# Kernel tuning notes

Measured on AMD Instinct MI355X. Metric: run time of the kernel, lower is better.

Reference implementation:

```python
import jax, jax.numpy as jnp
import numpy as np


def _gcn_norm(edge_index, num_nodes):
    # PyG GCNConv(normalize=True): add self-loops, symmetric normalization.
    src, dst = edge_index[0], edge_index[1]
    loop = jnp.arange(num_nodes, dtype=src.dtype)
    src = jnp.concatenate([src, loop])
    dst = jnp.concatenate([dst, loop])
    ones = jnp.ones(src.shape[0], dtype=jnp.float32)
    deg = jax.ops.segment_sum(ones, dst, num_segments=num_nodes)
    dinv = jax.lax.rsqrt(jnp.maximum(deg, 1.0))  # deg >= 1 with self-loops
    norm = dinv[src] * dinv[dst]  # [E+N]
    return src, dst, norm


def _gcn_layer(x, W, b, src, dst, norm, num_nodes):
    h = x @ W                                   # [N, out]
    msg = norm[:, None] * h[src]                # [E+N, out] gather
    agg = jax.ops.segment_sum(msg, dst, num_segments=num_nodes)  # scatter-add
    return agg + b


def setup_inputs() -> dict:
    key = jax.random.key(0)
    ks = jax.random.split(key, 8)
    N, E, F = 50000, 400000, 128
    v = jax.random.normal(ks[0], (N, F), dtype=jnp.float32)
    edge_index = jax.random.randint(ks[1], (2, E), 0, N, dtype=jnp.int64)
    def glorot(k, fan_in, fan_out):
        s = jnp.sqrt(6.0 / (fan_in + fan_out))
        return jax.random.uniform(k, (fan_in, fan_out), jnp.float32, -s, s)
    return {
        "v": v,
        "edge_index": edge_index,
        "W1": glorot(ks[2], F, 128), "b1": jnp.zeros((128,), jnp.float32),
        "W2": glorot(ks[3], 128, 256), "b2": jnp.zeros((256,), jnp.float32),
        "W3": glorot(ks[4], 256, 512), "b3": jnp.zeros((512,), jnp.float32),
    }


def reference(v, edge_index, W1, b1, W2, b2, W3, b3):
    N = v.shape[0]
    src, dst, norm = _gcn_norm(edge_index, N)
    x = jax.nn.relu(_gcn_layer(v, W1, b1, src, dst, norm, N))
    x = jax.nn.relu(_gcn_layer(x, W2, b2, src, dst, norm, N))
    x = jax.nn.relu(_gcn_layer(x, W3, b3, src, dst, norm, N))
    return x
```

## Files before the change

kernel.cpp:

```cpp
#include <hip/hip_runtime.h>
#include <hip/hip_bf16.h>
#include <stdint.h>

static constexpr int NN = 50000;
static constexpr int NE = 400000;
static constexpr int NB = (NN + 1023) / 1024;

typedef __attribute__((ext_vector_type(8))) short bf16x8;
typedef __attribute__((ext_vector_type(8))) unsigned short u16x8;
typedef __attribute__((ext_vector_type(4))) float f32x4;

__device__ inline ushort f2bf(float f) {
    __hip_bfloat16 b = __float2bfloat16(f);
    return *reinterpret_cast<ushort*>(&b);
}
__device__ inline float bfu2f(ushort u) {
    unsigned x = (unsigned)u << 16;
    return __builtin_bit_cast(float, x);
}

__device__ __forceinline__ void gload16(const void* g, void* l) {
    __builtin_amdgcn_global_load_lds(
        (const __attribute__((address_space(1))) void*)g,
        (__attribute__((address_space(3))) void*)l, 16, 0, 0);
}


__global__ void k_count(const int* __restrict__ ei, unsigned* __restrict__ cnt) {
    int e = blockIdx.x * blockDim.x + threadIdx.x;
    if (e < NE) atomicAdd(&cnt[ei[NE + e]], 1u);
}

__global__ void k_dinv(const unsigned* __restrict__ cnt, float* __restrict__ dinv) {
    int i = blockIdx.x * blockDim.x + threadIdx.x;
    if (i < NN) dinv[i] = rsqrtf((float)(cnt[i] + 1u));
}


__global__ __launch_bounds__(1024) void k_scan1(const unsigned* __restrict__ cnt,
                                                unsigned* __restrict__ offs,
                                                unsigned* __restrict__ bsum) {
    __shared__ unsigned sh[1024];
    int i = blockIdx.x * 1024 + (int)threadIdx.x;
    unsigned v = (i < NN) ? cnt[i] : 0u;
    sh[threadIdx.x] = v;
    __syncthreads();
    #pragma unroll
    for (int off = 1; off < 1024; off <<= 1) {
        unsigned add = (threadIdx.x >= (unsigned)off) ? sh[threadIdx.x - off] : 0u;
        __syncthreads();
        sh[threadIdx.x] += add;
        __syncthreads();
    }
    if (i < NN) offs[i] = sh[threadIdx.x] - v;
    if (threadIdx.x == 1023) bsum[blockIdx.x] = sh[1023];
}

__global__ void k_scan2(const unsigned* __restrict__ bsum, unsigned* __restrict__ boff,
                        unsigned* __restrict__ offs) {
    if (threadIdx.x == 0) {
        unsigned acc = 0;
        for (int b = 0; b < NB; ++b) { boff[b] = acc; acc += bsum[b]; }
        offs[NN] = acc;
    }
}

__global__ __launch_bounds__(1024) void k_scan3(unsigned* __restrict__ offs,
                                                const unsigned* __restrict__ boff) {
    int i = blockIdx.x * 1024 + (int)threadIdx.x;
    if (i < NN) offs[i] += boff[blockIdx.x];
}

__global__ void k_fill(const int* __restrict__ ei, const unsigned* __restrict__ offs,
                       unsigned* __restrict__ cursor, const float* __restrict__ dinv,
                       unsigned* __restrict__ csr_src, float* __restrict__ csr_w) {
    int e = blockIdx.x * blockDim.x + threadIdx.x;
    if (e < NE) {
        int s = ei[e];
        int d = ei[NE + e];
        unsigned pos = offs[d] + atomicAdd(&cursor[d], 1u);
        csr_src[pos] = (unsigned)s;
        csr_w[pos] = dinv[s] * dinv[d];
    }
}


__global__ void k_castW(const float* __restrict__ W, ushort* __restrict__ Wt, int K, int N) {
    int i = blockIdx.x * 256 + (int)threadIdx.x;
    if (i >= K * N) return;
    int k = i / N, n = i - k * N;
    Wt[n * K + k] = f2bf(W[i]);
}


__global__ void k_castV(const float* __restrict__ v, ushort* __restrict__ vb, int n4) {
    int i = blockIdx.x * 256 + (int)threadIdx.x;
    if (i >= n4) return;
    float4 f = *reinterpret_cast<const float4*>(v + (size_t)i * 4);
    *reinterpret_cast<ushort4*>(vb + (size_t)i * 4) =
        make_ushort4(f2bf(f.x), f2bf(f.y), f2bf(f.z), f2bf(f.w));
}


template <int VEC>
__global__ __launch_bounds__(256) void k_aggregate(
        const ushort* __restrict__ x, ushort* __restrict__ y,
        const unsigned* __restrict__ offs, const unsigned* __restrict__ csr_src,
        const float* __restrict__ csr_w, const float* __restrict__ dinv) {
    const int F = 64 * VEC;
    constexpr int LPR = (VEC == 2) ? 16 : 32;
    constexpr int NEP = 64 / LPR;
    constexpr int U = 8 / NEP;
    int node = blockIdx.x * 4 + ((int)threadIdx.x >> 6);
    int lane = (int)threadIdx.x & 63;
    if (node >= NN) return;
    int h = lane / LPR;
    int sl = lane % LPR;

    float di = dinv[node];
    float sw = (h == 0) ? di * di : 0.f;
    float acc[8];
    {
        u16x8 u = *reinterpret_cast<const u16x8*>(x + (size_t)node * F + sl * 8);
        #pragma unroll
        for (int j = 0; j < 8; ++j) acc[j] = sw * bfu2f(u[j]);
    }

    unsigned beg = offs[node], end = offs[node + 1];
    unsigned e = beg + h;
    for (; e + NEP * (U - 1) < end; e += NEP * U) {
        unsigned s[U]; float w[U]; u16x8 u[U];
        #pragma unroll
        for (int k = 0; k < U; ++k) { s[k] = csr_src[e + NEP * k]; w[k] = csr_w[e + NEP * k]; }
        #pragma unroll
        for (int k = 0; k < U; ++k)
            u[k] = *reinterpret_cast<const u16x8*>(x + (size_t)s[k] * F + sl * 8);
        #pragma unroll
        for (int k = 0; k < U; ++k)
            #pragma unroll
            for (int j = 0; j < 8; ++j) acc[j] = fmaf(w[k], bfu2f(u[k][j]), acc[j]);
    }
    for (; e < end; e += NEP) {
        unsigned s0 = csr_src[e];
        float w0 = csr_w[e];
        u16x8 u0 = *reinterpret_cast<const u16x8*>(x + (size_t)s0 * F + sl * 8);
        #pragma unroll
        for (int j = 0; j < 8; ++j) acc[j] = fmaf(w0, bfu2f(u0[j]), acc[j]);
    }

    #pragma unroll
    for (int j = 0; j < 8; ++j) {
        acc[j] += __shfl_xor(acc[j], 32);
        if constexpr (LPR == 16) acc[j] += __shfl_xor(acc[j], 16);
    }

    if (h == 0) {
        ushort hh[8];
        #pragma unroll
        for (int j = 0; j < 8; ++j) hh[j] = f2bf(acc[j]);
        *reinterpret_cast<u16x8*>(y + (size_t)node * F + sl * 8) =
            *reinterpret_cast<u16x8*>(hh);
    }
}


template <int NT, int SC, bool OUTB>
__global__ __launch_bounds__(256, 4) void k_gemm7(
        const ushort* __restrict__ Ah, const ushort* __restrict__ Wt,
        const float* __restrict__ bias, void* __restrict__ Cout, int M, int N) {
    constexpr int K = NT * 32;
    constexpr int CHT = (NT > 2) ? 2 : NT;
    constexpr int NCH = NT / CHT;
    __shared__ __align__(16) float smem[4352];
    short* sB = (short*)smem;

    int nwg = (int)gridDim.x;
    int bid = (int)blockIdx.x;
    int q = nwg >> 3, r = nwg & 7;
    int xcd = bid & 7, seq = bid >> 3;
    int swz = (xcd < r ? xcd * (q + 1) : r * (q + 1) + (xcd - r) * q) + seq;
    int bx = swz % SC, by = swz / SC;
    int col0 = bx * 128, row0 = by * 128;

    int tid = (int)threadIdx.x;
    int w = tid >> 6, lane = tid & 63;
    int wr = w >> 1, wc = w & 1;
    int r16 = lane & 15, kg = lane >> 4;

    size_t aoff[4];
    #pragma unroll
    for (int mi = 0; mi < 4; ++mi) {
        int row = row0 + wr * 64 + mi * 16 + r16;
        if (row >= M) row = M - 1;
        aoff[mi] = (size_t)row * K + kg * 8;
    }

    f32x4 acc[4][4] = {};
    bf16x8 ah[3][4];

    #pragma unroll
    for (int mi = 0; mi < 4; ++mi)
        ah[0][mi] = *reinterpret_cast<const bf16x8*>(Ah + aoff[mi]);
    if constexpr (NT > 1) {
        #pragma unroll
        for (int mi = 0; mi < 4; ++mi)
            ah[1][mi] = *reinterpret_cast<const bf16x8*>(Ah + aoff[mi] + 32);
    }

    #pragma unroll
    for (int kc = 0; kc < NCH; ++kc) {
        if (kc) __syncthreads();
        #pragma unroll
        for (int i = 0; i < CHT * 2; ++i) {
            int c = i * 256 + tid;
            int tl = c >> 9, ckg = (c >> 7) & 3, n = c & 127;
            gload16(Wt + (size_t)(col0 + n) * K + (kc * CHT + tl) * 32 + ckg * 8,
                    sB + c * 8);
        }
        __syncthreads();

        #pragma unroll
        for (int t = 0; t < CHT; ++t) {
            const int tg = kc * CHT + t;
            const int cur = tg % 3;
            if (tg + 2 < NT) {
                const int nxt = (tg + 2) % 3;
                #pragma unroll
                for (int mi = 0; mi < 4; ++mi)
                    ah[nxt][mi] = *reinterpret_cast<const bf16x8*>(Ah + aoff[mi] + (tg + 2) * 32);
            }
            bf16x8 bb[4];
            #pragma unroll
            for (int ni = 0; ni < 4; ++ni)
                bb[ni] = *reinterpret_cast<const bf16x8*>(
                    sB + ((t * 4 + kg) * 128 + wc * 64 + ni * 16 + r16) * 8);
            #pragma unroll
            for (int ni = 0; ni < 4; ++ni)
                #pragma unroll
                for (int mi = 0; mi < 4; ++mi)
                    acc[mi][ni] = __builtin_amdgcn_mfma_f32_16x16x32_bf16(ah[cur][mi], bb[ni], acc[mi][ni], 0, 0, 0);
        }
    }

    __syncthreads();
    float* ep = smem + w * (16 * 68);
    int crow0 = (lane >> 4) * 4;
    int ccol = lane & 15;
    int rb = row0 + wr * 64;
    int cb = col0 + wc * 64;
    int rl0 = lane >> 4;
    int cl = (lane & 15) * 4;
    float4 bv = *reinterpret_cast<const float4*>(&bias[cb + cl]);
    #pragma unroll
    for (int mi = 0; mi < 4; ++mi) {
        #pragma unroll
        for (int ni = 0; ni < 4; ++ni)
            #pragma unroll
            for (int j = 0; j < 4; ++j)
                ep[(crow0 + j) * 68 + ni * 16 + ccol] = acc[mi][ni][j];
        #pragma unroll
        for (int s = 0; s < 4; ++s) {
            int rl = s * 4 + rl0;
            int row = rb + mi * 16 + rl;
            if (row < M) {
                float4 vv = *reinterpret_cast<const float4*>(ep + rl * 68 + cl);
                float4 o;
                o.x = fmaxf(vv.x + bv.x, 0.f);
                o.y = fmaxf(vv.y + bv.y, 0.f);
                o.z = fmaxf(vv.z + bv.z, 0.f);
                o.w = fmaxf(vv.w + bv.w, 0.f);
                if constexpr (OUTB) {
                    *reinterpret_cast<ushort4*>((ushort*)Cout + (size_t)row * N + cb + cl) =
                        make_ushort4(f2bf(o.x), f2bf(o.y), f2bf(o.z), f2bf(o.w));
                } else {
                    f32x4 ov = {o.x, o.y, o.z, o.w};
                    __builtin_nontemporal_store(
                        ov, reinterpret_cast<f32x4*>((float*)Cout + (size_t)row * N + cb + cl));
                }
            }
        }
    }
}


extern "C" void kernel_launch(void* const* d_in, const int* in_sizes, int n_in,
                              void* d_out, int out_size, void* d_ws, size_t ws_size,
                              hipStream_t stream) {
    const float* v  = (const float*)d_in[0];
    const int* ei   = (const int*)d_in[1];
    const float* W1 = (const float*)d_in[2];
    const float* b1 = (const float*)d_in[3];
    const float* W2 = (const float*)d_in[4];
    const float* b2 = (const float*)d_in[5];
    const float* W3 = (const float*)d_in[6];
    const float* b3 = (const float*)d_in[7];
    float* out = (float*)d_out;

    char* ws = (char*)d_ws;
    size_t off = 0;
    auto alloc = [&](size_t bytes) {
        void* p = ws + off;
        off = (off + bytes + 255) & ~(size_t)255;
        return p;
    };
    unsigned* cnt    = (unsigned*)(ws + 0);
    unsigned* cursor = (unsigned*)(ws + (size_t)NN * 4);
    ushort* Wt1 = (ushort*)ws;
    ushort* Wt2 = Wt1 + 128 * 128;
    off = ((size_t)NN * 8 + 255) & ~(size_t)255;
    unsigned* offs    = (unsigned*)alloc((size_t)(NN + 1) * 4);
    float*    dinv    = (float*)alloc((size_t)NN * 4);
    unsigned* bsum    = (unsigned*)alloc((size_t)NB * 4);
    unsigned* boff    = (unsigned*)alloc((size_t)NB * 4);
    unsigned* csr_src = (unsigned*)alloc((size_t)NE * 4);
    float*    csr_w   = (float*)alloc((size_t)NE * 4);
    ushort* Wt3 = (ushort*)csr_src;
    ushort* aggA = (ushort*)alloc((size_t)NN * 256 * 2);
    ushort* vb   = (ushort*)alloc((size_t)NN * 128 * 2);
    ushort* xb   = (ushort*)alloc((size_t)NN * 256 * 2);

    hipMemsetAsync(cnt, 0, (size_t)NN * 8, stream);

    k_count<<<(NE + 255) / 256, 256, 0, stream>>>(ei, cnt);
    k_dinv<<<(NN + 255) / 256, 256, 0, stream>>>(cnt, dinv);
    k_scan1<<<NB, 1024, 0, stream>>>(cnt, offs, bsum);
    k_scan2<<<1, 64, 0, stream>>>(bsum, boff, offs);
    k_scan3<<<NB, 1024, 0, stream>>>(offs, boff);
    k_fill<<<(NE + 255) / 256, 256, 0, stream>>>(ei, offs, cursor, dinv, csr_src, csr_w);

    k_castW<<<(128 * 128 + 255) / 256, 256, 0, stream>>>(W1, Wt1, 128, 128);
    k_castW<<<(128 * 256 + 255) / 256, 256, 0, stream>>>(W2, Wt2, 128, 256);
    k_castV<<<(NN * 128 / 4 + 255) / 256, 256, 0, stream>>>(v, vb, NN * 128 / 4);

    int aggGrid = (NN + 3) / 4;
    int gr = (NN + 127) / 128;

    k_aggregate<2><<<aggGrid, 256, 0, stream>>>(vb, aggA, offs, csr_src, csr_w, dinv);
    k_gemm7<4, 1, true><<<gr * 1, 256, 0, stream>>>(aggA, Wt1, b1, xb, NN, 128);

    k_aggregate<2><<<aggGrid, 256, 0, stream>>>(xb, aggA, offs, csr_src, csr_w, dinv);
    k_gemm7<4, 2, true><<<gr * 2, 256, 0, stream>>>(aggA, Wt2, b2, xb, NN, 256);

    k_aggregate<4><<<aggGrid, 256, 0, stream>>>(xb, aggA, offs, csr_src, csr_w, dinv);
    k_castW<<<(256 * 512 + 255) / 256, 256, 0, stream>>>(W3, Wt3, 256, 512);
    k_gemm7<8, 4, false><<<gr * 4, 256, 0, stream>>>(aggA, Wt3, b3, out, NN, 512);
}
```

Baseline: 233.0 us.

## Fuse prelude kernels and double-buffer weight tiles in GEMM

```diff
diff --git a/kernel.cpp b/kernel.cpp
--- a/kernel.cpp
+++ b/kernel.cpp
@@ -5,6 +5,11 @@
 static constexpr int NN = 50000;
 static constexpr int NE = 400000;
 static constexpr int NB = (NN + 1023) / 1024;
+
+static constexpr int PB_CNT = (NE + 255) / 256;
+static constexpr int PB_CV  = (NN * 128 / 4 + 255) / 256;
+static constexpr int PB_W1  = (128 * 128 + 255) / 256;
+static constexpr int PB_W2  = (128 * 256 + 255) / 256;
 
 typedef __attribute__((ext_vector_type(8))) short bf16x8;
 typedef __attribute__((ext_vector_type(8))) unsigned short u16x8;
@@ -26,23 +31,50 @@
 }
 
 
-__global__ void k_count(const int* __restrict__ ei, unsigned* __restrict__ cnt) {
-    int e = blockIdx.x * blockDim.x + threadIdx.x;
-    if (e < NE) atomicAdd(&cnt[ei[NE + e]], 1u);
-}
-
-__global__ void k_dinv(const unsigned* __restrict__ cnt, float* __restrict__ dinv) {
-    int i = blockIdx.x * blockDim.x + threadIdx.x;
-    if (i < NN) dinv[i] = rsqrtf((float)(cnt[i] + 1u));
+__global__ void k_prelude(const int* __restrict__ ei, unsigned* __restrict__ cnt,
+                          const float* __restrict__ v, ushort* __restrict__ vb,
+                          const float* __restrict__ W1, ushort* __restrict__ Wt1,
+                          const float* __restrict__ W2, ushort* __restrict__ Wt2) {
+    int b = blockIdx.x;
+    int tid = (int)threadIdx.x;
+    if (b < PB_CNT) {
+        int e = b * 256 + tid;
+        if (e < NE) atomicAdd(&cnt[ei[NE + e]], 1u);
+    } else if (b < PB_CNT + PB_CV) {
+        int i = (b - PB_CNT) * 256 + tid;
+        if (i < NN * 128 / 4) {
+            float4 f = *reinterpret_cast<const float4*>(v + (size_t)i * 4);
+            *reinterpret_cast<ushort4*>(vb + (size_t)i * 4) =
+                make_ushort4(f2bf(f.x), f2bf(f.y), f2bf(f.z), f2bf(f.w));
+        }
+    } else if (b < PB_CNT + PB_CV + PB_W1) {
+        int i = (b - PB_CNT - PB_CV) * 256 + tid;
+        int k = i >> 7, n = i & 127;
+        Wt1[n * 128 + k] = f2bf(W1[i]);
+    } else {
+        int i = (b - PB_CNT - PB_CV - PB_W1) * 256 + tid;
+        int k = i >> 8, n = i & 255;
+        Wt2[n * 128 + k] = f2bf(W2[i]);
+    }
+}
+
+
+__global__ void k_castW(const float* __restrict__ W, ushort* __restrict__ Wt, int K, int N) {
+    int i = blockIdx.x * 256 + (int)threadIdx.x;
+    if (i >= K * N) return;
+    int k = i / N, n = i - k * N;
+    Wt[n * K + k] = f2bf(W[i]);
 }
 
 
 __global__ __launch_bounds__(1024) void k_scan1(const unsigned* __restrict__ cnt,
                                                 unsigned* __restrict__ offs,
-                                                unsigned* __restrict__ bsum) {
+                                                unsigned* __restrict__ bsum,
+                                                float* __restrict__ dinv) {
     __shared__ unsigned sh[1024];
     int i = blockIdx.x * 1024 + (int)threadIdx.x;
     unsigned v = (i < NN) ? cnt[i] : 0u;
+    if (i < NN) dinv[i] = rsqrtf((float)(v + 1u));
     sh[threadIdx.x] = v;
     __syncthreads();
     #pragma unroll
@@ -82,23 +114,6 @@
         csr_src[pos] = (unsigned)s;
         csr_w[pos] = dinv[s] * dinv[d];
     }
-}
-
-
-__global__ void k_castW(const float* __restrict__ W, ushort* __restrict__ Wt, int K, int N) {
-    int i = blockIdx.x * 256 + (int)threadIdx.x;
-    if (i >= K * N) return;
-    int k = i / N, n = i - k * N;
-    Wt[n * K + k] = f2bf(W[i]);
-}
-
-
-__global__ void k_castV(const float* __restrict__ v, ushort* __restrict__ vb, int n4) {
-    int i = blockIdx.x * 256 + (int)threadIdx.x;
-    if (i >= n4) return;
-    float4 f = *reinterpret_cast<const float4*>(v + (size_t)i * 4);
-    *reinterpret_cast<ushort4*>(vb + (size_t)i * 4) =
-        make_ushort4(f2bf(f.x), f2bf(f.y), f2bf(f.z), f2bf(f.w));
 }
 
 
@@ -165,13 +180,13 @@
 
 
 template <int NT, int SC, bool OUTB>
-__global__ __launch_bounds__(256, 4) void k_gemm7(
+__global__ __launch_bounds__(256, 4) void k_gemm9(
         const ushort* __restrict__ Ah, const ushort* __restrict__ Wt,
         const float* __restrict__ bias, void* __restrict__ Cout, int M, int N) {
     constexpr int K = NT * 32;
-    constexpr int CHT = (NT > 2) ? 2 : NT;
+    constexpr int CHT = 2;
     constexpr int NCH = NT / CHT;
-    __shared__ __align__(16) float smem[4352];
+    __shared__ __align__(16) float smem[8192];
     short* sB = (short*)smem;
 
     int nwg = (int)gridDim.x;
@@ -195,30 +210,34 @@
         aoff[mi] = (size_t)row * K + kg * 8;
     }
 
-    f32x4 acc[4][4] = {};
-    bf16x8 ah[3][4];
-
-    #pragma unroll
-    for (int mi = 0; mi < 4; ++mi)
-        ah[0][mi] = *reinterpret_cast<const bf16x8*>(Ah + aoff[mi]);
-    if constexpr (NT > 1) {
-        #pragma unroll
-        for (int mi = 0; mi < 4; ++mi)
-            ah[1][mi] = *reinterpret_cast<const bf16x8*>(Ah + aoff[mi] + 32);
-    }
-
-    #pragma unroll
-    for (int kc = 0; kc < NCH; ++kc) {
-        if (kc) __syncthreads();
+    auto stage = [&](int b, int kc) {
+        short* dst = sB + b * 8192;
         #pragma unroll
         for (int i = 0; i < CHT * 2; ++i) {
             int c = i * 256 + tid;
             int tl = c >> 9, ckg = (c >> 7) & 3, n = c & 127;
             gload16(Wt + (size_t)(col0 + n) * K + (kc * CHT + tl) * 32 + ckg * 8,
-                    sB + c * 8);
+                    dst + c * 8);
         }
-        __syncthreads();
-
+    };
+
+    f32x4 acc[4][4] = {};
+    bf16x8 ah[3][4];
+
+    #pragma unroll
+    for (int mi = 0; mi < 4; ++mi)
+        ah[0][mi] = *reinterpret_cast<const bf16x8*>(Ah + aoff[mi]);
+    #pragma unroll
+    for (int mi = 0; mi < 4; ++mi)
+        ah[1][mi] = *reinterpret_cast<const bf16x8*>(Ah + aoff[mi] + 32);
+
+    stage(0, 0);
+    __syncthreads();
+
+    #pragma unroll
+    for (int kc = 0; kc < NCH; ++kc) {
+        if (kc + 1 < NCH) stage((kc + 1) & 1, kc + 1);
+        const short* sb = sB + (kc & 1) * 8192;
         #pragma unroll
         for (int t = 0; t < CHT; ++t) {
             const int tg = kc * CHT + t;
@@ -233,16 +252,16 @@
             #pragma unroll
             for (int ni = 0; ni < 4; ++ni)
                 bb[ni] = *reinterpret_cast<const bf16x8*>(
-                    sB + ((t * 4 + kg) * 128 + wc * 64 + ni * 16 + r16) * 8);
+                    sb + ((t * 4 + kg) * 128 + wc * 64 + ni * 16 + r16) * 8);
             #pragma unroll
             for (int ni = 0; ni < 4; ++ni)
                 #pragma unroll
                 for (int mi = 0; mi < 4; ++mi)
                     acc[mi][ni] = __builtin_amdgcn_mfma_f32_16x16x32_bf16(ah[cur][mi], bb[ni], acc[mi][ni], 0, 0, 0);
         }
-    }
-
-    __syncthreads();
+        __syncthreads();
+    }
+
     float* ep = smem + w * (16 * 68);
     int crow0 = (lane >> 4) * 4;
     int ccol = lane & 15;
@@ -305,9 +324,9 @@
     };
     unsigned* cnt    = (unsigned*)(ws + 0);
     unsigned* cursor = (unsigned*)(ws + (size_t)NN * 4);
-    ushort* Wt1 = (ushort*)ws;
-    ushort* Wt2 = Wt1 + 128 * 128;
     off = ((size_t)NN * 8 + 255) & ~(size_t)255;
+    ushort* Wt1 = (ushort*)alloc(128 * 128 * 2);
+    ushort* Wt2 = (ushort*)alloc(128 * 256 * 2);
     unsigned* offs    = (unsigned*)alloc((size_t)(NN + 1) * 4);
     float*    dinv    = (float*)alloc((size_t)NN * 4);
     unsigned* bsum    = (unsigned*)alloc((size_t)NB * 4);
@@ -321,27 +340,23 @@
 
     hipMemsetAsync(cnt, 0, (size_t)NN * 8, stream);
 
-    k_count<<<(NE + 255) / 256, 256, 0, stream>>>(ei, cnt);
-    k_dinv<<<(NN + 255) / 256, 256, 0, stream>>>(cnt, dinv);
-    k_scan1<<<NB, 1024, 0, stream>>>(cnt, offs, bsum);
+    k_prelude<<<PB_CNT + PB_CV + PB_W1 + PB_W2, 256, 0, stream>>>(
+        ei, cnt, v, vb, W1, Wt1, W2, Wt2);
+    k_scan1<<<NB, 1024, 0, stream>>>(cnt, offs, bsum, dinv);
     k_scan2<<<1, 64, 0, stream>>>(bsum, boff, offs);
     k_scan3<<<NB, 1024, 0, stream>>>(offs, boff);
     k_fill<<<(NE + 255) / 256, 256, 0, stream>>>(ei, offs, cursor, dinv, csr_src, csr_w);
 
-    k_castW<<<(128 * 128 + 255) / 256, 256, 0, stream>>>(W1, Wt1, 128, 128);
-    k_castW<<<(128 * 256 + 255) / 256, 256, 0, stream>>>(W2, Wt2, 128, 256);
-    k_castV<<<(NN * 128 / 4 + 255) / 256, 256, 0, stream>>>(v, vb, NN * 128 / 4);
-
     int aggGrid = (NN + 3) / 4;
     int gr = (NN + 127) / 128;
 
     k_aggregate<2><<<aggGrid, 256, 0, stream>>>(vb, aggA, offs, csr_src, csr_w, dinv);
-    k_gemm7<4, 1, true><<<gr * 1, 256, 0, stream>>>(aggA, Wt1, b1, xb, NN, 128);
+    k_gemm9<4, 1, true><<<gr * 1, 256, 0, stream>>>(aggA, Wt1, b1, xb, NN, 128);
 
     k_aggregate<2><<<aggGrid, 256, 0, stream>>>(xb, aggA, offs, csr_src, csr_w, dinv);
-    k_gemm7<4, 2, true><<<gr * 2, 256, 0, stream>>>(aggA, Wt2, b2, xb, NN, 256);
+    k_gemm9<4, 2, true><<<gr * 2, 256, 0, stream>>>(aggA, Wt2, b2, xb, NN, 256);
 
     k_aggregate<4><<<aggGrid, 256, 0, stream>>>(xb, aggA, offs, csr_src, csr_w, dinv);
     k_castW<<<(256 * 512 + 255) / 256, 256, 0, stream>>>(W3, Wt3, 256, 512);
-    k_gemm7<8, 4, false><<<gr * 4, 256, 0, stream>>>(aggA, Wt3, b3, out, NN, 512);
-}
+    k_gemm9<8, 4, false><<<gr * 4, 256, 0, stream>>>(aggA, Wt3, b3, out, NN, 512);
+}
```

Result: faster. 223.8 us (-3.9%).
